# Performance work log

Measured on AMD Instinct MI355X. Metric: run time of the kernel, lower is better.

The kernel has to match this reference:

```python
import jax, jax.numpy as jnp
import numpy as np

N = 30000      # nodes
D = 512        # nhid
E = 300000     # edges (before self-loops)
P_FEAT = 0.5   # feature dropout (F.dropout, training=True)
P_ATT = 0.6    # GATConv attention dropout
NEG_SLOPE = 0.2
SCALE = 1.0    # PairNorm scale


def setup_inputs() -> dict:
    key = jax.random.key(0)
    k1, k2, k3, k4, k5, k6 = jax.random.split(key, 6)
    x = jax.random.normal(k1, (N, D), dtype=jnp.float32)
    edge_index = jax.random.randint(k2, (2, E), 0, N, dtype=jnp.int32)
    # GATConv params (heads=1): lin weight, att_src/att_dst vectors, bias
    W = jax.random.normal(k3, (D, D), dtype=jnp.float32) * 0.05
    att_src = jax.random.normal(k4, (D,), dtype=jnp.float32) * 0.05
    att_dst = jax.random.normal(k5, (D,), dtype=jnp.float32) * 0.05
    bias = jax.random.normal(k6, (D,), dtype=jnp.float32) * 0.05
    return {"x": x, "edge_index": edge_index, "W": W,
            "att_src": att_src, "att_dst": att_dst, "bias": bias}


def reference(x, edge_index, W, att_src, att_dst, bias):
    # deterministic dropout masks (module runs with training=True)
    dk = jax.random.key(42)
    k_feat, k_att = jax.random.split(dk)

    # F.dropout(x, 0.5, training=True)
    keep = jax.random.bernoulli(k_feat, 1.0 - P_FEAT, x.shape)
    x = jnp.where(keep, x / (1.0 - P_FEAT), jnp.float32(0.0))

    # GATConv(heads=1): linear transform
    h = x @ W                                     # [N, D]

    # add self-loops (PyG default add_self_loops=True)
    src, dst = edge_index[0], edge_index[1]
    loop = jnp.arange(N, dtype=src.dtype)
    src = jnp.concatenate([src, loop])            # [E+N]
    dst = jnp.concatenate([dst, loop])

    # per-edge attention logits: LeakyReLU(a_src . h_j + a_dst . h_i)
    a_s = h @ att_src                             # [N]
    a_d = h @ att_dst                             # [N]
    e = jax.nn.leaky_relu(a_s[src] + a_d[dst], NEG_SLOPE)   # [E+N]

    # segment softmax over incoming edges of each dst node
    m = jax.ops.segment_max(e, dst, num_segments=N)
    m = jnp.where(jnp.isfinite(m), m, jnp.float32(0.0))
    ee = jnp.exp(e - m[dst])
    s = jax.ops.segment_sum(ee, dst, num_segments=N)
    alpha = ee / (s[dst] + 1e-16)                 # [E+N]

    # attention dropout p=0.6
    keep_a = jax.random.bernoulli(k_att, 1.0 - P_ATT, alpha.shape)
    alpha = jnp.where(keep_a, alpha / (1.0 - P_ATT), jnp.float32(0.0))

    # scatter-aggregate weighted messages, add bias
    out = jax.ops.segment_sum(alpha[:, None] * h[src], dst, num_segments=N) + bias

    # PairNorm 'PN': center columns, scale by mean row norm
    out = out - jnp.mean(out, axis=0)
    rownorm_mean = jnp.sqrt(1e-6 + jnp.mean(jnp.sum(out * out, axis=1)))
    out = SCALE * out / rownorm_mean

    return jax.nn.relu(out)
```

## Files before the change

### kernel.cpp

```cpp
#include <hip/hip_runtime.h>
#include <stdint.h>
#include <math.h>


#define N_NODES 30000
#define MPAD    30080
#define DIM     512
#define NEDGE   300000
#define ETOT    330000
#define AGG_BLOCKS 7500
#define RED_BLOCKS 60
#define RED_ROWS   125

#define GEMM_BLOCKS 940
#define CVT_BLOCKS  256
#define DROP_BLOCKS 7520
#define HIST_BLOCKS 1290
#define DOT_BLOCKS  118

#define STILES 118

typedef unsigned int u32;
typedef unsigned short u16;

typedef __attribute__((ext_vector_type(8))) short bf16x8;
typedef __attribute__((ext_vector_type(4))) float f32x4;

__host__ __device__ __forceinline__ void threefry2x32(u32 k0, u32 k1, u32 x0, u32 x1,
                                                      u32& o0, u32& o1) {
  u32 ks2 = k0 ^ k1 ^ 0x1BD11BDAu;
#define TF_R(r) { x0 += x1; x1 = (x1 << r) | (x1 >> (32 - r)); x1 ^= x0; }
  x0 += k0; x1 += k1;
  TF_R(13) TF_R(15) TF_R(26) TF_R(6)
  x0 += k1; x1 += ks2 + 1u;
  TF_R(17) TF_R(29) TF_R(16) TF_R(24)
  x0 += ks2; x1 += k0 + 2u;
  TF_R(13) TF_R(15) TF_R(26) TF_R(6)
  x0 += k0; x1 += k1 + 3u;
  TF_R(17) TF_R(29) TF_R(16) TF_R(24)
  x0 += k1; x1 += ks2 + 4u;
  TF_R(13) TF_R(15) TF_R(26) TF_R(6)
  x0 += ks2; x1 += k0 + 5u;
#undef TF_R
  o0 = x0; o1 = x1;
}

__device__ __forceinline__ u32 tf_fold(u32 k0, u32 k1, u32 idx) {
  u32 a, b;
  threefry2x32(k0, k1, 0u, idx, a, b);
  return a ^ b;
}

__device__ __forceinline__ float bf2f(u32 bits16) {
  return __uint_as_float(bits16 << 16);
}
__device__ __forceinline__ u16 f2bf(float f) {
  u32 u = __float_as_uint(f);
  return (u16)((u + 0x7fffu + ((u >> 16) & 1u)) >> 16);
}

__global__ __launch_bounds__(256) void k_pre(const float* __restrict__ W,
                                             u16* __restrict__ Wt,
                                             const float* __restrict__ x,
                                             u16* __restrict__ xd,
                                             const int* __restrict__ ei,
                                             int* __restrict__ counts,
                                             u32 kf0, u32 kf1) {
  __shared__ u16 tile[32][33];
  int b = blockIdx.x;
  if (b < CVT_BLOCKS) {
    int bk = (b & 15) * 32, bn = (b >> 4) * 32;
    int c = threadIdx.x & 31, r = threadIdx.x >> 5;
#pragma unroll
    for (int rr = 0; rr < 32; rr += 8)
      tile[r + rr][c] = f2bf(W[(size_t)(bk + r + rr) * DIM + bn + c]);
    __syncthreads();
#pragma unroll
    for (int rr = 0; rr < 32; rr += 8)
      Wt[(size_t)(bn + r + rr) * DIM + bk + c] = tile[c][r + rr];
  } else if (b < CVT_BLOCKS + DROP_BLOCKS) {
    size_t gid = (size_t)(b - CVT_BLOCKS) * 256 + threadIdx.x;
    size_t i0 = gid * 8;
    if (i0 < (size_t)MPAD * DIM) {
      uint4 o = make_uint4(0u, 0u, 0u, 0u);
      if (i0 < (size_t)N_NODES * DIM) {
        float4 v0 = *(const float4*)(x + i0);
        float4 v1 = *(const float4*)(x + i0 + 4);
        float xv[8] = {v0.x, v0.y, v0.z, v0.w, v1.x, v1.y, v1.z, v1.w};
        u32 res[4];
#pragma unroll
        for (int p = 0; p < 4; p++) {
          u32 b0 = tf_fold(kf0, kf1, (u32)i0 + 2 * p);
          u32 b1 = tf_fold(kf0, kf1, (u32)i0 + 2 * p + 1);
          u32 r0 = (b0 >> 31) ? 0u : (u32)f2bf(2.0f * xv[2 * p]);
          u32 r1 = (b1 >> 31) ? 0u : (u32)f2bf(2.0f * xv[2 * p + 1]);
          res[p] = r0 | (r1 << 16);
        }
        o = make_uint4(res[0], res[1], res[2], res[3]);
      }
      *(uint4*)(xd + i0) = o;
    }
  } else {
    int i = (b - CVT_BLOCKS - DROP_BLOCKS) * 256 + threadIdx.x;
    if (i < ETOT) {
      int d = (i < NEDGE) ? ei[NEDGE + i] : (i - NEDGE);
      atomicAdd(&counts[d], 1);
    }
  }
}

__global__ __launch_bounds__(256) void k_gemm(const u16* __restrict__ A,
                                              const u16* __restrict__ B,
                                              u16* __restrict__ H,
                                              const float* __restrict__ atts,
                                              const float* __restrict__ attd,
                                              float* __restrict__ aspart,
                                              float* __restrict__ adpart,
                                              const int* __restrict__ counts,
                                              int* __restrict__ off,
                                              int* __restrict__ cursor) {
  __shared__ __align__(16) u16 lA[128 * 32];
  __shared__ __align__(16) u16 lB[128 * 32];

  if (blockIdx.x == 0) {
    int* tsum = (int*)lA;
    int tid = threadIdx.x, lane = tid & 63, wid = tid >> 6;

    for (int t0 = wid; t0 < STILES; t0 += 32) {
      int4 v[8];
#pragma unroll
      for (int b = 0; b < 8; b++) {
        int t = t0 + b * 4;
        int i = t * 256 + lane * 4;
        if (t < STILES) {
          if (i + 4 <= N_NODES) {
            v[b] = *(const int4*)(counts + i);
          } else {
            v[b].x = (i     < N_NODES) ? counts[i]     : 0;
            v[b].y = (i + 1 < N_NODES) ? counts[i + 1] : 0;
            v[b].z = (i + 2 < N_NODES) ? counts[i + 2] : 0;
            v[b].w = (i + 3 < N_NODES) ? counts[i + 3] : 0;
          }
        } else {
          v[b] = make_int4(0, 0, 0, 0);
        }
      }
#pragma unroll
      for (int b = 0; b < 8; b++) {
        int t = t0 + b * 4;
        if (t < STILES) {
          int s = v[b].x + v[b].y + v[b].z + v[b].w;
#pragma unroll
          for (int d = 1; d < 64; d <<= 1) s += __shfl_xor(s, d);
          if (lane == 0) tsum[t] = s;
        }
      }
    }
    __syncthreads();

    if (wid == 0) {
      int carry = 0;
#pragma unroll
      for (int r = 0; r < 2; r++) {
        int idx = r * 64 + lane;
        int vv = (idx < STILES) ? tsum[idx] : 0;
        int x = vv;
#pragma unroll
        for (int d = 1; d < 64; d <<= 1) {
          int y = __shfl_up(x, d);
          if (lane >= d) x += y;
        }
        if (idx < STILES) tsum[idx] = x - vv + carry;
        carry += __shfl(x, 63);
      }
    }
    __syncthreads();

    for (int t0 = wid; t0 < STILES; t0 += 32) {
      int4 v[8];
#pragma unroll
      for (int b = 0; b < 8; b++) {
        int t = t0 + b * 4;
        int i = t * 256 + lane * 4;
        if (t < STILES) {
          if (i + 4 <= N_NODES) {
            v[b] = *(const int4*)(counts + i);
          } else {
            v[b].x = (i     < N_NODES) ? counts[i]     : 0;
            v[b].y = (i + 1 < N_NODES) ? counts[i + 1] : 0;
            v[b].z = (i + 2 < N_NODES) ? counts[i + 2] : 0;
            v[b].w = (i + 3 < N_NODES) ? counts[i + 3] : 0;
          }
        } else {
          v[b] = make_int4(0, 0, 0, 0);
        }
      }
#pragma unroll
      for (int b = 0; b < 8; b++) {
        int t = t0 + b * 4;
        if (t >= STILES) continue;
        int i = t * 256 + lane * 4;
        int s4 = v[b].x + v[b].y + v[b].z + v[b].w;
        int x = s4;
#pragma unroll
        for (int d = 1; d < 64; d <<= 1) {
          int y = __shfl_up(x, d);
          if (lane >= d) x += y;
        }
        int base = tsum[t] + (x - s4);
        int4 e;
        e.x = base;
        e.y = base + v[b].x;
        e.z = e.y + v[b].y;
        e.w = e.z + v[b].z;
        if (i + 4 <= N_NODES) {
          *(int4*)(off + i) = e;
          *(int4*)(cursor + i) = e;
        } else {
          if (i     < N_NODES) { off[i]     = e.x; cursor[i]     = e.x; }
          if (i + 1 < N_NODES) { off[i + 1] = e.y; cursor[i + 1] = e.y; }
          if (i + 2 < N_NODES) { off[i + 2] = e.z; cursor[i + 2] = e.z; }
          if (i + 3 < N_NODES) { off[i + 3] = e.w; cursor[i + 3] = e.w; }
        }
      }
    }
    if (tid == 0) off[N_NODES] = ETOT;
    return;
  }

  const int g = blockIdx.x - 1;
  const int xcd = g & 7, gi = g >> 3;
  const int wrk = (xcd < 4 ? xcd * 118 : 472 + (xcd - 4) * 117) + gi;

  const int bn = (wrk & 3) * 128;
  const int bm = (wrk >> 2) * 128;
  const int tid = threadIdx.x;
  const int wave = tid >> 6, lane = tid & 63;
  const int quad = lane >> 4, l16 = lane & 15;
  const int wrow = (wave & 1) * 64, wcol = (wave >> 1) * 64;

  f32x4 acc[4][4] = {};
  const int srow = tid >> 2;
  const int scq  = (tid & 3) * 8;

  for (int k0 = 0; k0 < DIM; k0 += 32) {
    uint4 va0 = *(const uint4*)(A + (size_t)(bm + srow) * DIM + k0 + scq);
    uint4 va1 = *(const uint4*)(A + (size_t)(bm + 64 + srow) * DIM + k0 + scq);
    uint4 vb0 = *(const uint4*)(B + (size_t)(bn + srow) * DIM + k0 + scq);
    uint4 vb1 = *(const uint4*)(B + (size_t)(bn + 64 + srow) * DIM + k0 + scq);
    __syncthreads();
    *(uint4*)(lA + srow * 32 + scq) = va0;
    *(uint4*)(lA + (64 + srow) * 32 + scq) = va1;
    *(uint4*)(lB + srow * 32 + scq) = vb0;
    *(uint4*)(lB + (64 + srow) * 32 + scq) = vb1;
    __syncthreads();

    bf16x8 af[4], bfr[4];
#pragma unroll
    for (int i = 0; i < 4; i++)
      af[i] = *(const bf16x8*)(lA + (wrow + i * 16 + l16) * 32 + quad * 8);
#pragma unroll
    for (int j = 0; j < 4; j++)
      bfr[j] = *(const bf16x8*)(lB + (wcol + j * 16 + l16) * 32 + quad * 8);
#pragma unroll
    for (int i = 0; i < 4; i++)
#pragma unroll
      for (int j = 0; j < 4; j++)
        acc[i][j] = __builtin_amdgcn_mfma_f32_16x16x32_bf16(af[i], bfr[j], acc[i][j], 0, 0, 0);
  }

#pragma unroll
  for (int i = 0; i < 4; i++) {
#pragma unroll
    for (int r = 0; r < 4; r++) {
      int row = bm + wrow + i * 16 + quad * 4 + r;
      u16* hp = H + (size_t)row * DIM + bn + wcol + l16;
#pragma unroll
      for (int j = 0; j < 4; j++) hp[j * 16] = f2bf(acc[i][j][r]);
    }
  }

  float as_j[4], ad_j[4];
#pragma unroll
  for (int j = 0; j < 4; j++) {
    int col = bn + wcol + j * 16 + l16;
    as_j[j] = atts[col];
    ad_j[j] = attd[col];
  }
  int slot = ((bn >> 7) << 1) + (wcol >> 6);
#pragma unroll
  for (int i = 0; i < 4; i++) {
#pragma unroll
    for (int r = 0; r < 4; r++) {
      float ps = acc[i][0][r] * as_j[0] + acc[i][1][r] * as_j[1]
               + acc[i][2][r] * as_j[2] + acc[i][3][r] * as_j[3];
      float pd = acc[i][0][r] * ad_j[0] + acc[i][1][r] * ad_j[1]
               + acc[i][2][r] * ad_j[2] + acc[i][3][r] * ad_j[3];
#pragma unroll
      for (int d = 1; d < 16; d <<= 1) {
        ps += __shfl_xor(ps, d);
        pd += __shfl_xor(pd, d);
      }
      int row = bm + wrow + i * 16 + quad * 4 + r;
      if (l16 == 0) {
        aspart[slot * MPAD + row] = ps;
        adpart[slot * MPAD + row] = pd;
      }
    }
  }
}

__global__ __launch_bounds__(256) void k_mid(const float* __restrict__ aspart,
                                             const float* __restrict__ adpart,
                                             float* __restrict__ a_s,
                                             float* __restrict__ a_d,
                                             const int* __restrict__ ei,
                                             int* __restrict__ cursor,
                                             int* __restrict__ perm) {
  int b = blockIdx.x;
  if (b < DOT_BLOCKS) {
    int i = b * 256 + threadIdx.x;
    if (i < N_NODES) {
      float s = 0.f, d = 0.f;
#pragma unroll
      for (int k = 0; k < 8; k++) {
        s += aspart[k * MPAD + i];
        d += adpart[k * MPAD + i];
      }
      a_s[i] = s;
      a_d[i] = d;
    }
  } else {
    int i = (b - DOT_BLOCKS) * 256 + threadIdx.x;
    if (i < ETOT) {
      int d = (i < NEDGE) ? ei[NEDGE + i] : (i - NEDGE);
      int slot = atomicAdd(&cursor[d], 1);
      perm[slot] = i;
    }
  }
}

__global__ __launch_bounds__(256) void k_aggregate(
    const int* __restrict__ ei, const int* __restrict__ off, const int* __restrict__ perm,
    const float* __restrict__ a_s, const float* __restrict__ a_d,
    const u16* __restrict__ h, const float* __restrict__ bias,
    u16* __restrict__ oa, float* __restrict__ colpart,
    float* __restrict__ ssqpart, u32 ka0, u32 ka1) {
  __shared__ float lbuf[4][512];
  int wid = threadIdx.x >> 6;
  int node = blockIdx.x * 4 + wid;
  int lane = threadIdx.x & 63;
  int beg = off[node], end = off[node + 1];
  int deg = end - beg;
  float adn = a_d[node];

  float acc[8] = {0.f, 0.f, 0.f, 0.f, 0.f, 0.f, 0.f, 0.f};

  if (deg <= 64) {
    int idx = beg + lane;
    bool valid = idx < end;
    int s = 0;
    float lg = -3.0e38f;
    u32 keepbits = 0;
    if (valid) {
      int eid = perm[idx];
      s = (eid < NEDGE) ? ei[eid] : (eid - NEDGE);
      lg = a_s[s] + adn;
      lg = (lg < 0.f) ? 0.2f * lg : lg;
      keepbits = tf_fold(ka0, ka1, (u32)eid);
    }
    float mx = lg;
#pragma unroll
    for (int d = 1; d < 64; d <<= 1) mx = fmaxf(mx, __shfl_xor(mx, d));
    float ee = valid ? expf(lg - mx) : 0.f;
    float ssum = ee;
#pragma unroll
    for (int d = 1; d < 64; d <<= 1) ssum += __shfl_xor(ssum, d);
    float inv_s = 2.5f / (ssum + 1e-16f);
    float w = (valid && ((keepbits >> 9) < 3355444u)) ? ee * inv_s : 0.f;

    for (int j = 0; j < deg; j++) {
      float wj = __shfl(w, j);
      if (wj != 0.f) {
        int sj = __shfl(s, j);
        uint4 hv = *(const uint4*)(h + (size_t)sj * DIM + lane * 8);
        u32 hw[4] = {hv.x, hv.y, hv.z, hv.w};
#pragma unroll
        for (int p = 0; p < 4; p++) {
          acc[2 * p]     += wj * bf2f(hw[p] & 0xffffu);
          acc[2 * p + 1] += wj * bf2f(hw[p] >> 16);
        }
      }
    }
  } else {
    float mx = -3.0e38f;
    for (int base = beg; base < end; base += 64) {
      int idx = base + lane;
      if (idx < end) {
        int eid = perm[idx];
        int s = (eid < NEDGE) ? ei[eid] : (eid - NEDGE);
        float lg = a_s[s] + adn;
        lg = (lg < 0.f) ? 0.2f * lg : lg;
        mx = fmaxf(mx, lg);
      }
    }
#pragma unroll
    for (int d = 1; d < 64; d <<= 1) mx = fmaxf(mx, __shfl_xor(mx, d));
    float ssum = 0.f;
    for (int base = beg; base < end; base += 64) {
      int idx = base + lane;
      if (idx < end) {
        int eid = perm[idx];
        int s = (eid < NEDGE) ? ei[eid] : (eid - NEDGE);
        float lg = a_s[s] + adn;
        lg = (lg < 0.f) ? 0.2f * lg : lg;
        ssum += expf(lg - mx);
      }
    }
#pragma unroll
    for (int d = 1; d < 64; d <<= 1) ssum += __shfl_xor(ssum, d);
    float inv_s = 2.5f / (ssum + 1e-16f);
    for (int base = beg; base < end; base += 64) {
      int idx = base + lane;
      float w = 0.f; int s = 0;
      if (idx < end) {
        int eid = perm[idx];
        s = (eid < NEDGE) ? ei[eid] : (eid - NEDGE);
        float lg = a_s[s] + adn;
        lg = (lg < 0.f) ? 0.2f * lg : lg;
        float ee = expf(lg - mx);
        u32 bits = tf_fold(ka0, ka1, (u32)eid);
        if ((bits >> 9) < 3355444u) w = ee * inv_s;
      }
      int cnt = min(64, end - base);
      for (int j = 0; j < cnt; j++) {
        float wj = __shfl(w, j);
        if (wj != 0.f) {
          int sj = __shfl(s, j);
          uint4 hv = *(const uint4*)(h + (size_t)sj * DIM + lane * 8);
          u32 hw[4] = {hv.x, hv.y, hv.z, hv.w};
#pragma unroll
          for (int p = 0; p < 4; p++) {
            acc[2 * p]     += wj * bf2f(hw[p] & 0xffffu);
            acc[2 * p + 1] += wj * bf2f(hw[p] >> 16);
          }
        }
      }
    }
  }

  float4 b0 = *(const float4*)(bias + lane * 8);
  float4 b1 = *(const float4*)(bias + lane * 8 + 4);
  float bb[8] = {b0.x, b0.y, b0.z, b0.w, b1.x, b1.y, b1.z, b1.w};
  u32 res[4];
  float vq[8];
#pragma unroll
  for (int p = 0; p < 4; p++) {
    u16 q0 = f2bf(acc[2 * p]     + bb[2 * p]);
    u16 q1 = f2bf(acc[2 * p + 1] + bb[2 * p + 1]);
    res[p] = (u32)q0 | ((u32)q1 << 16);
    vq[2 * p]     = bf2f(q0);
    vq[2 * p + 1] = bf2f(q1);
  }
  *(uint4*)(oa + (size_t)node * DIM + lane * 8) = make_uint4(res[0], res[1], res[2], res[3]);
  *(float4*)&lbuf[wid][lane * 8]     = make_float4(vq[0], vq[1], vq[2], vq[3]);
  *(float4*)&lbuf[wid][lane * 8 + 4] = make_float4(vq[4], vq[5], vq[6], vq[7]);
  __syncthreads();

  int t = threadIdx.x;
  float s0 = 0.f, s1 = 0.f, ssl = 0.f;
#pragma unroll
  for (int w = 0; w < 4; w++) {
    float a = lbuf[w][t], b = lbuf[w][t + 256];
    s0 += a; s1 += b;
    ssl = fmaf(a, a, ssl);
    ssl = fmaf(b, b, ssl);
  }
  colpart[(size_t)blockIdx.x * 512 + t]       = s0;
  colpart[(size_t)blockIdx.x * 512 + 256 + t] = s1;
#pragma unroll
  for (int d = 1; d < 64; d <<= 1) ssl += __shfl_xor(ssl, d);
  __shared__ float wss[4];
  if ((t & 63) == 0) wss[t >> 6] = ssl;
  __syncthreads();
  if (t == 0) ssqpart[blockIdx.x] = wss[0] + wss[1] + wss[2] + wss[3];
}

__global__ __launch_bounds__(256) void k_redstats(const float* __restrict__ colpart,
                                                  const float* __restrict__ ssqpart,
                                                  float* __restrict__ colsum,
                                                  double* __restrict__ ssq) {
  int b = blockIdx.x;
  int t = threadIdx.x;
  int r0 = b * RED_ROWS;
  float s0 = 0.f, s1 = 0.f;
  for (int r = r0; r < r0 + RED_ROWS; r++) {
    s0 += colpart[(size_t)r * 512 + t];
    s1 += colpart[(size_t)r * 512 + 256 + t];
  }
  atomicAdd(&colsum[t], s0);
  atomicAdd(&colsum[t + 256], s1);
  float sl = (t < RED_ROWS) ? ssqpart[r0 + t] : 0.f;
#pragma unroll
  for (int d = 1; d < 64; d <<= 1) sl += __shfl_xor(sl, d);
  __shared__ float w4[4];
  if ((t & 63) == 0) w4[t >> 6] = sl;
  __syncthreads();
  if (t == 0) atomicAdd(ssq, (double)(w4[0] + w4[1] + w4[2] + w4[3]));
}

__global__ __launch_bounds__(512) void k_finalize(const float* __restrict__ colsum,
                                                  const double* __restrict__ ssq,
                                                  float* __restrict__ mu,
                                                  float* __restrict__ invp) {
  __shared__ double sred[8];
  int j = threadIdx.x;
  float m = colsum[j] * (1.0f / 30000.0f);
  mu[j] = m;
  double p = (double)m * (double)m;
#pragma unroll
  for (int d = 1; d < 64; d <<= 1) p += __shfl_xor(p, d);
  int lane = j & 63, wid = j >> 6;
  if (lane == 0) sred[wid] = p;
  __syncthreads();
  if (j == 0) {
    double smu2 = 0.0;
#pragma unroll
    for (int w = 0; w < 8; w++) smu2 += sred[w];
    double centered = ssq[0] - 30000.0 * smu2;
    double mean = centered * (1.0 / 30000.0);
    if (!(mean >= 0.0)) mean = 0.0;
    float rn = sqrtf(1e-6f + (float)mean);
    invp[0] = 1.0f / rn;
  }
}

__global__ __launch_bounds__(256) void k_finalout(const u16* __restrict__ oa,
                                                  const float* __restrict__ mu,
                                                  const float* __restrict__ invp,
                                                  float* __restrict__ out) {
  size_t gid = (size_t)blockIdx.x * 256 + threadIdx.x;
  size_t i0 = gid * 8;
  if (i0 >= (size_t)N_NODES * DIM) return;
  float inv = invp[0];
  int j = (int)(i0 & (DIM - 1));
  uint4 v = *(const uint4*)(oa + i0);
  u32 w[4] = {v.x, v.y, v.z, v.w};
  float o[8];
#pragma unroll
  for (int p = 0; p < 4; p++) {
    float z0 = (bf2f(w[p] & 0xffffu) - mu[j + 2 * p]) * inv;
    float z1 = (bf2f(w[p] >> 16)     - mu[j + 2 * p + 1]) * inv;
    o[2 * p]     = (z0 < 0.f) ? 0.f : z0;
    o[2 * p + 1] = (z1 < 0.f) ? 0.f : z1;
  }
  *(float4*)(out + i0)     = make_float4(o[0], o[1], o[2], o[3]);
  *(float4*)(out + i0 + 4) = make_float4(o[4], o[5], o[6], o[7]);
}

extern "C" void kernel_launch(void* const* d_in, const int* in_sizes, int n_in,
                              void* d_out, int out_size, void* d_ws, size_t ws_size,
                              hipStream_t stream) {
  const float* x    = (const float*)d_in[0];
  const int*   ei   = (const int*)d_in[1];
  const float* W    = (const float*)d_in[2];
  const float* atts = (const float*)d_in[3];
  const float* attd = (const float*)d_in[4];
  const float* bias = (const float*)d_in[5];
  float* out = (float*)d_out;
  char* ws = (char*)d_ws;

  u16*   xd      = (u16*)(ws + 0);
  u16*   oa      = (u16*)(ws + 0);
  float* aspart  = (float*)(ws + 32000000);
  float* adpart  = (float*)(ws + 33000000);
  u16*   h       = (u16*)(ws + 61440000);
  u16*   Wt      = (u16*)(ws + 92241920);
  float* a_s     = (float*)(ws + 92766208);
  float* a_d     = (float*)(ws + 92886272);
  int*   counts  = (int*)(ws + 93006336);
  int*   offs    = (int*)(ws + 93126400);
  int*   cursor  = (int*)(ws + 93246464);
  int*   perm    = (int*)(ws + 93366528);
  float* colsum  = (float*)(ws + 94686528);
  float* mu      = (float*)(ws + 94688576);
  double* ssq    = (double*)(ws + 94690624);
  float* invp    = (float*)(ws + 94690688);

  float* colpart = out;
  float* ssqpart = out + (size_t)AGG_BLOCKS * 512;

  u32 kf0, kf1, ka0, ka1;
  threefry2x32(0u, 42u, 0u, 0u, kf0, kf1);
  threefry2x32(0u, 42u, 0u, 1u, ka0, ka1);

  hipMemsetAsync(counts, 0, 120064, stream);
  hipMemsetAsync((void*)colsum, 0, 4224, stream);

  k_pre<<<CVT_BLOCKS + DROP_BLOCKS + HIST_BLOCKS, 256, 0, stream>>>(
      W, Wt, x, xd, ei, counts, kf0, kf1);
  k_gemm<<<GEMM_BLOCKS + 1, 256, 0, stream>>>(xd, Wt, h, atts, attd,
                                              aspart, adpart, counts, offs, cursor);
  k_mid<<<DOT_BLOCKS + HIST_BLOCKS, 256, 0, stream>>>(aspart, adpart, a_s, a_d,
                                                      ei, cursor, perm);
  k_aggregate<<<AGG_BLOCKS, 256, 0, stream>>>(ei, offs, perm, a_s, a_d, h, bias,
                                              oa, colpart, ssqpart, ka0, ka1);
  k_redstats<<<RED_BLOCKS, 256, 0, stream>>>(colpart, ssqpart, colsum, ssq);
  k_finalize<<<1, 512, 0, stream>>>(colsum, ssq, mu, invp);
  k_finalout<<<7500, 256, 0, stream>>>(oa, mu, invp, out);
}
```

Baseline: 271.7 us.

## Batch gather loads in aggregation and fold finalize into redstats via last-block reduction

The aggregation inner loop now processes neighbors in groups of four, issuing all four row gathers before accumulating. This exposes more memory-level parallelism in the latency-bound gather. Separately, the separate finalize kernel and the colsum memset are removed. Redstats blocks write partials, and the last block to arrive (tracked by an atomic counter that k_pre resets) computes mu and the inverse norm. This saves a launch and a memset but adds threadfence and atomic-counter synchronization.

```diff
diff --git a/kernel.cpp b/kernel.cpp
--- a/kernel.cpp
+++ b/kernel.cpp
@@ -65,9 +65,11 @@
                                              u16* __restrict__ xd,
                                              const int* __restrict__ ei,
                                              int* __restrict__ counts,
+                                             unsigned int* __restrict__ done,
                                              u32 kf0, u32 kf1) {
   __shared__ u16 tile[32][33];
   int b = blockIdx.x;
+  if (b == 0 && threadIdx.x == 0) *done = 0u;
   if (b < CVT_BLOCKS) {
     int bk = (b & 15) * 32, bn = (b >> 4) * 32;
     int c = threadIdx.x & 31, r = threadIdx.x >> 5;
@@ -379,16 +381,40 @@
     float inv_s = 2.5f / (ssum + 1e-16f);
     float w = (valid && ((keepbits >> 9) < 3355444u)) ? ee * inv_s : 0.f;
 
-    for (int j = 0; j < deg; j++) {
-      float wj = __shfl(w, j);
-      if (wj != 0.f) {
-        int sj = __shfl(s, j);
-        uint4 hv = *(const uint4*)(h + (size_t)sj * DIM + lane * 8);
-        u32 hw[4] = {hv.x, hv.y, hv.z, hv.w};
+    int j = 0;
+    for (; j + 4 <= deg; j += 4) {
+      float wj[4]; int sj[4]; uint4 hv[4];
+#pragma unroll
+      for (int bq = 0; bq < 4; bq++) {
+        wj[bq] = __shfl(w, j + bq);
+        sj[bq] = __shfl(s, j + bq);
+      }
+#pragma unroll
+      for (int bq = 0; bq < 4; bq++)
+        if (wj[bq] != 0.f)
+          hv[bq] = *(const uint4*)(h + (size_t)sj[bq] * DIM + lane * 8);
+#pragma unroll
+      for (int bq = 0; bq < 4; bq++) {
+        if (wj[bq] != 0.f) {
+          u32 hw[4] = {hv[bq].x, hv[bq].y, hv[bq].z, hv[bq].w};
+#pragma unroll
+          for (int p = 0; p < 4; p++) {
+            acc[2 * p]     += wj[bq] * bf2f(hw[p] & 0xffffu);
+            acc[2 * p + 1] += wj[bq] * bf2f(hw[p] >> 16);
+          }
+        }
+      }
+    }
+    for (; j < deg; j++) {
+      float wjv = __shfl(w, j);
+      if (wjv != 0.f) {
+        int sjv = __shfl(s, j);
+        uint4 hvv = *(const uint4*)(h + (size_t)sjv * DIM + lane * 8);
+        u32 hw[4] = {hvv.x, hvv.y, hvv.z, hvv.w};
 #pragma unroll
         for (int p = 0; p < 4; p++) {
-          acc[2 * p]     += wj * bf2f(hw[p] & 0xffffu);
-          acc[2 * p + 1] += wj * bf2f(hw[p] >> 16);
+          acc[2 * p]     += wjv * bf2f(hw[p] & 0xffffu);
+          acc[2 * p + 1] += wjv * bf2f(hw[p] >> 16);
         }
       }
     }
@@ -488,8 +514,11 @@
 
 __global__ __launch_bounds__(256) void k_redstats(const float* __restrict__ colpart,
                                                   const float* __restrict__ ssqpart,
-                                                  float* __restrict__ colsum,
-                                                  double* __restrict__ ssq) {
+                                                  float* __restrict__ colpart2,
+                                                  double* __restrict__ ssqp2,
+                                                  unsigned int* __restrict__ done,
+                                                  float* __restrict__ mu,
+                                                  float* __restrict__ invp) {
   int b = blockIdx.x;
   int t = threadIdx.x;
   int r0 = b * RED_ROWS;
@@ -498,40 +527,53 @@
     s0 += colpart[(size_t)r * 512 + t];
     s1 += colpart[(size_t)r * 512 + 256 + t];
   }
-  atomicAdd(&colsum[t], s0);
-  atomicAdd(&colsum[t + 256], s1);
+  colpart2[(size_t)b * 512 + t]       = s0;
+  colpart2[(size_t)b * 512 + 256 + t] = s1;
   float sl = (t < RED_ROWS) ? ssqpart[r0 + t] : 0.f;
 #pragma unroll
   for (int d = 1; d < 64; d <<= 1) sl += __shfl_xor(sl, d);
   __shared__ float w4[4];
   if ((t & 63) == 0) w4[t >> 6] = sl;
   __syncthreads();
-  if (t == 0) atomicAdd(ssq, (double)(w4[0] + w4[1] + w4[2] + w4[3]));
-}
-
-__global__ __launch_bounds__(512) void k_finalize(const float* __restrict__ colsum,
-                                                  const double* __restrict__ ssq,
-                                                  float* __restrict__ mu,
-                                                  float* __restrict__ invp) {
-  __shared__ double sred[8];
-  int j = threadIdx.x;
-  float m = colsum[j] * (1.0f / 30000.0f);
-  mu[j] = m;
-  double p = (double)m * (double)m;
-#pragma unroll
-  for (int d = 1; d < 64; d <<= 1) p += __shfl_xor(p, d);
-  int lane = j & 63, wid = j >> 6;
-  if (lane == 0) sred[wid] = p;
+  if (t == 0) ssqp2[b] = (double)(w4[0] + w4[1] + w4[2] + w4[3]);
+
+  __threadfence();
   __syncthreads();
-  if (j == 0) {
-    double smu2 = 0.0;
-#pragma unroll
-    for (int w = 0; w < 8; w++) smu2 += sred[w];
-    double centered = ssq[0] - 30000.0 * smu2;
-    double mean = centered * (1.0 / 30000.0);
-    if (!(mean >= 0.0)) mean = 0.0;
-    float rn = sqrtf(1e-6f + (float)mean);
-    invp[0] = 1.0f / rn;
+  __shared__ unsigned int olds;
+  if (t == 0) olds = atomicAdd(done, 1u);
+  __syncthreads();
+  if (olds == RED_BLOCKS - 1) {
+    __threadfence();
+    float m0 = 0.f, m1 = 0.f;
+    for (int r = 0; r < RED_BLOCKS; r++) {
+      m0 += colpart2[(size_t)r * 512 + t];
+      m1 += colpart2[(size_t)r * 512 + 256 + t];
+    }
+    m0 *= (1.0f / 30000.0f);
+    m1 *= (1.0f / 30000.0f);
+    mu[t]       = m0;
+    mu[t + 256] = m1;
+    double p = (double)m0 * (double)m0 + (double)m1 * (double)m1;
+#pragma unroll
+    for (int d = 1; d < 64; d <<= 1) p += __shfl_xor(p, d);
+    __shared__ double sred[4];
+    __shared__ double ssqs;
+    if ((t & 63) == 0) sred[t >> 6] = p;
+    if (t < 64) {
+      double sq = (t < RED_BLOCKS) ? ssqp2[t] : 0.0;
+#pragma unroll
+      for (int d = 1; d < 64; d <<= 1) sq += __shfl_xor(sq, d);
+      if (t == 0) ssqs = sq;
+    }
+    __syncthreads();
+    if (t == 0) {
+      double smu2 = sred[0] + sred[1] + sred[2] + sred[3];
+      double centered = ssqs - 30000.0 * smu2;
+      double mean = centered * (1.0 / 30000.0);
+      if (!(mean >= 0.0)) mean = 0.0;
+      float rn = sqrtf(1e-6f + (float)mean);
+      invp[0] = 1.0f / rn;
+    }
   }
 }
 
@@ -574,6 +616,9 @@
   u16*   oa      = (u16*)(ws + 0);
   float* aspart  = (float*)(ws + 32000000);
   float* adpart  = (float*)(ws + 33000000);
+  float* colpart2 = (float*)(ws + 34000000);
+  double* ssqp2  = (double*)(ws + 34130000);
+  unsigned int* done = (unsigned int*)(ws + 34140000);
   u16*   h       = (u16*)(ws + 61440000);
   u16*   Wt      = (u16*)(ws + 92241920);
   float* a_s     = (float*)(ws + 92766208);
@@ -582,9 +627,7 @@
   int*   offs    = (int*)(ws + 93126400);
   int*   cursor  = (int*)(ws + 93246464);
   int*   perm    = (int*)(ws + 93366528);
-  float* colsum  = (float*)(ws + 94686528);
   float* mu      = (float*)(ws + 94688576);
-  double* ssq    = (double*)(ws + 94690624);
   float* invp    = (float*)(ws + 94690688);
 
   float* colpart = out;
@@ -595,17 +638,16 @@
   threefry2x32(0u, 42u, 0u, 1u, ka0, ka1);
 
   hipMemsetAsync(counts, 0, 120064, stream);
-  hipMemsetAsync((void*)colsum, 0, 4224, stream);
 
   k_pre<<<CVT_BLOCKS + DROP_BLOCKS + HIST_BLOCKS, 256, 0, stream>>>(
-      W, Wt, x, xd, ei, counts, kf0, kf1);
+      W, Wt, x, xd, ei, counts, done, kf0, kf1);
   k_gemm<<<GEMM_BLOCKS + 1, 256, 0, stream>>>(xd, Wt, h, atts, attd,
                                               aspart, adpart, counts, offs, cursor);
   k_mid<<<DOT_BLOCKS + HIST_BLOCKS, 256, 0, stream>>>(aspart, adpart, a_s, a_d,
                                                       ei, cursor, perm);
   k_aggregate<<<AGG_BLOCKS, 256, 0, stream>>>(ei, offs, perm, a_s, a_d, h, bias,
                                               oa, colpart, ssqpart, ka0, ka1);
-  k_redstats<<<RED_BLOCKS, 256, 0, stream>>>(colpart, ssqpart, colsum, ssq);
-  k_finalize<<<1, 512, 0, stream>>>(colsum, ssq, mu, invp);
+  k_redstats<<<RED_BLOCKS, 256, 0, stream>>>(colpart, ssqpart, colpart2, ssqp2,
+                                             done, mu, invp);
   k_finalout<<<7500, 256, 0, stream>>>(oa, mu, invp, out);
 }
```

Measured after the change: 271.2 us. Within noise of the previous version (-0.2%).
